# Kernel optimization log

Measured on AMD Instinct MI355X. Metric: run time of the kernel, lower is better.

## Reference

```python
import jax, jax.numpy as jnp
import numpy as np
from jax import lax

C = 256
HEADS = 8
HD = C // HEADS  # 32
D = 32  # max(L=32, C//16)
KERNELS = [1, 3, 5, 7]
EPS = 1e-5


def setup_inputs() -> dict:
    key = jax.random.key(0)
    ks = jax.random.split(key, 16)
    inp = {
        'x': jax.random.normal(ks[0], (8, C, 32, 32), jnp.float32),
        'qkv_w': jax.random.normal(ks[1], (3 * C, C), jnp.float32) * 0.05,
        'out_w': jax.random.normal(ks[2], (C, C), jnp.float32) * 0.05,
        'conv_w1': jax.random.normal(ks[3], (C, C, 1, 1), jnp.float32) * 0.05,
        'conv_w3': jax.random.normal(ks[4], (C, C, 3, 3), jnp.float32) * 0.05,
        'conv_w5': jax.random.normal(ks[5], (C, C, 5, 5), jnp.float32) * 0.05,
        'conv_w7': jax.random.normal(ks[6], (C, C, 7, 7), jnp.float32) * 0.05,
        'conv_b': jax.random.normal(ks[7], (4, C), jnp.float32) * 0.05,
        'bn_gamma': jax.random.uniform(ks[8], (4, C), jnp.float32, 0.5, 1.5),
        'bn_beta': jax.random.normal(ks[9], (4, C), jnp.float32) * 0.05,
        'bn_mean': jax.random.normal(ks[10], (4, C), jnp.float32) * 0.05,
        'bn_var': jax.random.uniform(ks[11], (4, C), jnp.float32, 0.5, 1.5),
        'fc_w': jax.random.normal(ks[12], (D, C), jnp.float32) * 0.05,
        'fc_b': jax.random.normal(ks[13], (D,), jnp.float32) * 0.05,
        'fcs_w': jax.random.normal(ks[14], (4, C, D), jnp.float32) * 0.05,
        'fcs_b': jax.random.normal(ks[15], (4, C), jnp.float32) * 0.05,
    }
    return inp


def _conv_bn_relu(x, w, b, g, beta, m, v):
    k = w.shape[-1]
    y = lax.conv_general_dilated(
        x, w, window_strides=(1, 1), padding=[(k // 2, k // 2)] * 2,
        dimension_numbers=('NCHW', 'OIHW', 'NCHW'))
    y = y + b[None, :, None, None]
    inv = g / jnp.sqrt(v + EPS)  # eval-mode batchnorm
    y = y * inv[None, :, None, None] + (beta - m * inv)[None, :, None, None]
    return jax.nn.relu(y)


def reference(x, qkv_w, out_w, conv_w1, conv_w3, conv_w5, conv_w7, conv_b,
              bn_gamma, bn_beta, bn_mean, bn_var, fc_w, fc_b, fcs_w, fcs_b):
    bsz, ch, ht, wd = x.shape
    n = ht * wd
    xf = x.reshape(bsz, ch, n)
    qkv = jnp.einsum('oc,bcn->bon', qkv_w, xf)  # [b, 3C, N] (1x1 conv)
    q, k, v = jnp.split(qkv, 3, axis=1)
    q = q.reshape(bsz, HEADS, HD, n)
    k = k.reshape(bsz, HEADS, HD, n)
    v = v.reshape(bsz, HEADS, HD, n)
    scale = 1.0 / np.sqrt(HD)
    scores = jnp.einsum('bhdi,bhdj->bhij', q, k) * scale  # [b,h,N,N]
    probs = jax.nn.softmax(scores, axis=-1)
    ctx = jnp.einsum('bhij,bhdj->bhdi', probs, v)  # [b,h,hd,N]
    ctx = ctx.reshape(bsz, ch, ht, wd)
    out = jnp.einsum('oc,bcn->bon', out_w, ctx.reshape(bsz, ch, n)).reshape(bsz, ch, ht, wd)

    ws = [conv_w1, conv_w3, conv_w5, conv_w7]
    feats = jnp.stack([
        _conv_bn_relu(out, ws[i], conv_b[i], bn_gamma[i], bn_beta[i], bn_mean[i], bn_var[i])
        for i in range(4)
    ], axis=0)  # [4, b, C, H, W]
    U = feats.sum(axis=0)
    S = U.mean(axis=(-2, -1))  # [b, C]
    Z = S @ fc_w.T + fc_b  # [b, D]
    logits = jnp.einsum('kcd,bd->kbc', fcs_w, Z) + fcs_b[:, None, :]  # [4,b,C]
    attn = jax.nn.softmax(logits, axis=0)[:, :, :, None, None]  # softmax over kernel branches
    V = (attn * feats).sum(axis=0)  # [b, C, H, W]
    return V
```

## Files before the change

### kernel.cpp

```cpp
#include <hip/hip_runtime.h>
#include <math.h>


typedef __attribute__((ext_vector_type(8))) short bf16x8;
typedef __attribute__((ext_vector_type(4))) float f32x4;

__device__ __forceinline__ ushort f2bf(float f) {
  uint32_t u = __float_as_uint(f);
  u += 0x7fffu + ((u >> 16) & 1u);
  return (ushort)(u >> 16);
}

__device__ __forceinline__ uint cvt_pk(float lo, float hi) {
  uint r;
  asm volatile("v_cvt_pk_bf16_f32 %0, %1, %2" : "=v"(r) : "v"(lo), "v"(hi));
  return r;
}


template <int KK>
__device__ __forceinline__ void repack_dev(const float* __restrict__ src,
                                           ushort* __restrict__ dst, int M, int co,
                                           char* smraw) {
  ushort(*t)[KK + 1] = (ushort(*)[KK + 1])smraw;
  int tid = threadIdx.x;
  for (int idx = tid; idx < 256 * KK; idx += 256) {
    int ci = idx / KK, k = idx - ci * KK;
    t[ci][k] = f2bf(src[(size_t)co * 256 * KK + idx]);
  }
  __syncthreads();
  for (int idx = tid; idx < 256 * KK; idx += 256) {
    int k = idx >> 8, ci = idx & 255;
    dst[((size_t)k * M + co) * 256 + ci] = t[ci][k];
  }
}

__device__ __forceinline__ void pad_dev(const float* __restrict__ src,
                                        ushort* __restrict__ dst, int y, int b,
                                        char* smraw) {
  ushort(*t)[258] = (ushort(*)[258])smraw;
  int tid = threadIdx.x;
  for (int u = 0; u < 32; ++u) {
    int idx = u * 256 + tid;
    int c = idx >> 5, p = idx & 31;
    t[p][c] = f2bf(src[(((size_t)b * 256 + c) << 10) + (y << 5) + p]);
  }
  __syncthreads();
  for (int u = 0; u < 32; ++u) {
    int idx = u * 256 + tid;
    int p = idx >> 8, c = idx & 255;
    dst[(((size_t)b * 38 + y + 3) * 38 + p + 3) * 256 + c] = t[p][c];
  }
}

__global__ __launch_bounds__(256) void prep_all(
    const float* __restrict__ qkv_w, const float* __restrict__ out_w,
    const float* __restrict__ cw1, const float* __restrict__ cw3,
    const float* __restrict__ cw5, const float* __restrict__ cw7,
    ushort* __restrict__ Wq, ushort* __restrict__ Wo, ushort* __restrict__ Wc,
    const float* __restrict__ x, ushort* __restrict__ P1,
    const float* __restrict__ cb, const float* __restrict__ g,
    const float* __restrict__ be, const float* __restrict__ mn,
    const float* __restrict__ v, float* __restrict__ binv, float* __restrict__ bb2) {
  __shared__ __align__(16) char sm[25600];
  int gx = blockIdx.x;
  if (gx < 768) repack_dev<1>(qkv_w, Wq, 768, gx, sm);
  else if (gx < 1024) repack_dev<1>(out_w, Wo, 256, gx - 768, sm);
  else if (gx < 1280) repack_dev<1>(cw1, Wc, 256, gx - 1024, sm);
  else if (gx < 1536) repack_dev<9>(cw3, Wc + 65536, 256, gx - 1280, sm);
  else if (gx < 1792) repack_dev<25>(cw5, Wc + 655360, 256, gx - 1536, sm);
  else if (gx < 2048) repack_dev<49>(cw7, Wc + 2293760, 256, gx - 1792, sm);
  else if (gx < 2304) pad_dev(x, P1, (gx - 2048) & 31, (gx - 2048) >> 5, sm);
  else if (gx == 2304) {
    int tid = threadIdx.x;
#pragma unroll
    for (int u = 0; u < 4; ++u) {
      int i = u * 256 + tid;
      float inv = g[i] * rsqrtf(v[i] + 1e-5f);
      binv[i] = inv;
      bb2[i] = be[i] + (cb[i] - mn[i]) * inv;
    }
  } else {
    int z = gx - 2305;
    int b = z >> 3;
    int part = z & 7;
    uint4* b4 = (uint4*)(P1 + (size_t)b * 369664);
    uint4 z4; z4.x = z4.y = z4.z = z4.w = 0u;
    for (int q = 0; q < 7; ++q) {
      int idx = q * 256 + threadIdx.x;
      if (idx < 1680) {
        int uidx = part * 1680 + idx;
        int p = uidx >> 5, ch = uidx & 31;
        int y, xx;
        if (p < 114) { y = p / 38; xx = p - y * 38; }
        else if (p < 306) {
          int r = p - 114; int ry = r / 6; int xi = r - ry * 6;
          y = 3 + ry; xx = xi < 3 ? xi : xi + 32;
        } else {
          int r = p - 306; int ry = r / 38; y = 35 + ry; xx = r - ry * 38;
        }
        b4[(y * 38 + xx) * 32 + ch] = z4;
      }
    }
  }
}

template <int MODE>
__device__ __forceinline__ void conv_core(
    const ushort* __restrict__ W, const ushort* __restrict__ X,
    float* __restrict__ outF, ushort* __restrict__ outU,
    int M, int KS, int b, int co0, int pxt, int cs0, int cs1, bool accum,
    char* smem) {
  const int R = KS >> 1;
  const int NT = KS * KS;
  const int NR = 4 + 2 * R;
  const int NPIX = NR * 38;
  char* Bs = smem;
  char* As = smem + 24320;
  const int tid = threadIdx.x;
  const int w = tid >> 6, l = tid & 63, lr = l & 15, sg = l >> 4;
  const int y0 = pxt * 4;
  const ushort* Xb = X + ((size_t)b * 38 + (y0 + 3 - R)) * 38 * 256;

  f32x4 acc[4][4] = {};

  auto stageA = [&](int t, int ci0, int bufsel) {
    const ushort* Wt = W + ((size_t)t * M + co0) * 256 + ci0;
    char* dbase = As + (bufsel << 13) + (w << 11);
#pragma unroll
    for (int u = 0; u < 2; ++u) {
      int idx16 = (w * 2 + u) * 64 + l;
      int co = idx16 >> 2, s = idx16 & 3;
      const ushort* src = Wt + (size_t)co * 256 + ((s ^ ((co >> 1) & 3)) << 3);
      __builtin_amdgcn_global_load_lds(
          (const __attribute__((address_space(1))) void*)src,
          (__attribute__((address_space(3))) void*)(dbase + (u << 10)), 16, 0, 0);
    }
  };

  int g = 0;
  stageA(0, cs0 << 5, 0);
  const int u_stg = (NPIX * 4 + 255) >> 8;
  for (int cs = cs0; cs < cs1; ++cs) {
    int ci0 = cs << 5;
    for (int u = 0; u < u_stg; ++u) {
      int idx = (u << 8) + tid;
      if (idx < NPIX * 4) {
        int pix = idx >> 2, s = idx & 3;
        int pr = pix / 38, pc = pix - pr * 38;
        const ushort* srcp = Xb + ((size_t)(pr * 38 + pc)) * 256 + ci0 +
                             ((s ^ ((pc >> 1) & 3)) << 3);
        __builtin_amdgcn_global_load_lds(
            (const __attribute__((address_space(1))) void*)srcp,
            (__attribute__((address_space(3))) void*)(Bs + (u << 12) + (w << 10)),
            16, 0, 0);
      }
    }
    __syncthreads();
    int dy = 0, dx = 0;
    for (int t = 0; t < NT; ++t) {
      bool staged = true;
      if (t + 1 < NT) stageA(t + 1, ci0, (g + 1) & 1);
      else if (cs + 1 < cs1) stageA(0, ci0 + 32, (g + 1) & 1);
      else staged = false;
      if (staged)
        asm volatile("s_waitcnt vmcnt(2)\n\ts_barrier" ::: "memory");
      else
        asm volatile("s_waitcnt vmcnt(0)\n\ts_barrier" ::: "memory");

      bf16x8 af[4], bfr[4];
      char* Ab = As + ((g & 1) << 13);
#pragma unroll
      for (int fa = 0; fa < 4; ++fa) {
        int co = (w & 1) * 64 + fa * 16 + lr;
        af[fa] = *(const bf16x8*)(Ab + (co << 6) + ((sg ^ ((co >> 1) & 3)) << 4));
      }
      int rowbase = (w >> 1) * 2 + dy;
      int cbase = dx + 3 - R + lr;
#pragma unroll
      for (int fp = 0; fp < 4; ++fp) {
        int lrow = rowbase + (fp >> 1);
        int pc = cbase + ((fp & 1) << 4);
        bfr[fp] = *(const bf16x8*)(Bs + ((lrow * 38 + pc) << 6) +
                                   ((sg ^ ((pc >> 1) & 3)) << 4));
      }
      __builtin_amdgcn_s_setprio(1);
#pragma unroll
      for (int fa = 0; fa < 4; ++fa)
#pragma unroll
        for (int fp = 0; fp < 4; ++fp)
          acc[fa][fp] = __builtin_amdgcn_mfma_f32_16x16x32_bf16(
              af[fa], bfr[fp], acc[fa][fp], 0, 0, 0);
      __builtin_amdgcn_s_setprio(0);
      ++g;
      if (++dx == KS) { dx = 0; ++dy; }
      asm volatile("s_barrier" ::: "memory");
    }
  }
  int coB = co0 + (w & 1) * 64;
  int pxB = pxt * 128 + (w >> 1) * 64;
#pragma unroll
  for (int fa = 0; fa < 4; ++fa) {
#pragma unroll
    for (int fp = 0; fp < 4; ++fp) {
      int px = pxB + (fp >> 1) * 32 + (fp & 1) * 16 + lr;
      int cobase = coB + fa * 16 + 4 * sg;
      f32x4 v4 = acc[fa][fp];
      if (MODE == 2) {
#pragma unroll
        for (int r = 0; r < 4; ++r) {
          int co = cobase + r;
          float* dst = &outF[((size_t)b * M + co) * 1024 + px];
          if (accum) unsafeAtomicAdd(dst, v4[r]);
          else *dst = v4[r];
        }
      } else if (MODE == 1) {
        int y = px >> 5, x = px & 31;
        ushort* dst = outU + ((size_t)(b * 38 + y + 3) * 38 + x + 3) * 256 + cobase;
        *(uint*)dst = cvt_pk(v4[0], v4[1]);
        *(uint*)(dst + 2) = cvt_pk(v4[2], v4[3]);
      } else {
        if (coB < 256) {
          int h = cobase >> 5, d = cobase & 31;
          ushort* dst = outU + ((size_t)(b * 8 + h) * 1024 + px) * 32 + d;
          const float sc = 0.17677669529663687f;
          *(uint*)dst = cvt_pk(v4[0] * sc, v4[1] * sc);
          *(uint*)(dst + 2) = cvt_pk(v4[2] * sc, v4[3] * sc);
        } else if (coB < 512) {
          int c2 = cobase - 256;
          int h = c2 >> 5, d = c2 & 31;
          ushort* dst = outU + 2097152 + ((size_t)(b * 8 + h) * 1024 + px) * 32 + d;
          *(uint*)dst = cvt_pk(v4[0], v4[1]);
          *(uint*)(dst + 2) = cvt_pk(v4[2], v4[3]);
        } else {
          int c2 = cobase - 512;
#pragma unroll
          for (int r = 0; r < 4; ++r)
            outU[4194304 + ((size_t)(b * 256 + c2 + r)) * 1024 + px] = f2bf(v4[r]);
        }
      }
    }
  }
}

__global__ __launch_bounds__(256, 2) void gemm_qkv(const ushort* __restrict__ W,
                                                   const ushort* __restrict__ X,
                                                   ushort* __restrict__ U) {
  __shared__ __align__(16) char smem[40704];
  int cot = blockIdx.x >> 3, pxt = blockIdx.x & 7, b = blockIdx.y;
  conv_core<0>(W, X, nullptr, U, 768, 1, b, cot * 128, pxt, 0, 8, false, smem);
}

__global__ __launch_bounds__(256, 2) void gemm_oproj(const ushort* __restrict__ W,
                                                     const ushort* __restrict__ X,
                                                     ushort* __restrict__ U,
                                                     float* __restrict__ fz) {
  __shared__ __align__(16) char smem[40704];
  int cot = blockIdx.x >> 3, pxt = blockIdx.x & 7, b = blockIdx.y;
  conv_core<1>(W, X, nullptr, U, 256, 1, b, cot * 128, pxt, 0, 8, false, smem);
  int blk = blockIdx.y * 16 + blockIdx.x;
  float4* dst = (float4*)fz + (size_t)blk * 12288;
  float4 z4 = {0.f, 0.f, 0.f, 0.f};
#pragma unroll
  for (int q = 0; q < 48; ++q) dst[q * 256 + threadIdx.x] = z4;
}

__global__ __launch_bounds__(256, 4) void conv_fused(const ushort* __restrict__ Wc,
                                                     const ushort* __restrict__ X,
                                                     float* __restrict__ feats) {
  __shared__ __align__(16) char smem[40704];
  int gx = blockIdx.x;
  int sub = gx & 127;
  int pxt = sub & 7, cot = (sub >> 3) & 1, b = sub >> 4;
  int br, cs0, cs1;
  if (gx < 512) {
    br = 3; int ch = gx >> 7; cs0 = ch * 2; cs1 = cs0 + 2;
  } else if (gx < 768) {
    br = 2; int ch = (gx >> 7) & 1; cs0 = ch * 4; cs1 = cs0 + 4;
  } else {
    br = 1; int ch = (gx >> 7) & 1; cs0 = ch * 4; cs1 = cs0 + 4;
  }
  const int ksarr[4] = {1, 3, 5, 7};
  const int wofs[4] = {0, 65536, 655360, 2293760};
  conv_core<2>(Wc + wofs[br], X, feats + (size_t)br * 2097152, nullptr, 256,
               ksarr[br], b, cot * 128, pxt, cs0, cs1, true, smem);
  if (gx >= 768 && gx < 896) {
    __syncthreads();
    conv_core<2>(Wc, X, feats, nullptr, 256, 1, b, cot * 128, pxt, 0, 8, false,
                 smem);
  }
}

__global__ __launch_bounds__(256, 2) void flash_attn(const ushort* __restrict__ QKV,
                                                     ushort* __restrict__ P2out) {
  __shared__ __align__(16) char smem[16384];
  const int tid = threadIdx.x, w = tid >> 6, l = tid & 63, lr = l & 15, sg = l >> 4;
  char* Ps = smem + (w << 12);
  int bh = blockIdx.y, b = bh >> 3, h = bh & 7;
  const ushort* QT = QKV + (size_t)bh * 32768;
  const ushort* KT = QKV + 2097152 + (size_t)bh * 32768;
  const ushort* VT = QKV + 4194304 + (size_t)(b * 256 + h * 32) * 1024;
  int ibase = blockIdx.x * 128 + w * 32;

  bf16x8 qf[2];
#pragma unroll
  for (int i16 = 0; i16 < 2; ++i16)
    qf[i16] = *(const bf16x8*)(QT + ((size_t)(ibase + i16 * 16 + lr)) * 32 + sg * 8);

  f32x4 oacc[4] = {};
  float mrow[2] = {-3e30f, -3e30f};
  float lrow[2] = {0.f, 0.f};

  const ushort* Krow = KT + (size_t)lr * 32 + sg * 8;
  const ushort* Vrow = VT + (size_t)lr * 1024 + sg * 8;

  bf16x8 k0[4], v0[4], k1[4], v1[4];
  auto LK = [&](int jb, bf16x8* kf) {
#pragma unroll
    for (int jt = 0; jt < 4; ++jt)
      kf[jt] = *(const bf16x8*)(Krow + ((size_t)jb + jt * 16) * 32);
  };
  auto LV = [&](int jb, bf16x8* vf) {
#pragma unroll
    for (int d16 = 0; d16 < 2; ++d16)
#pragma unroll
      for (int h2 = 0; h2 < 2; ++h2)
        vf[d16 * 2 + h2] =
            *(const bf16x8*)(Vrow + (size_t)d16 * 16384 + jb + h2 * 32);
  };

  auto body = [&](int jb, bf16x8* kc, bf16x8* vc, bf16x8* kn, bf16x8* vn) {
    if (jb + 64 < 1024) { LK(jb + 64, kn); LV(jb + 64, vn); }
    f32x4 sac[2][4] = {};
#pragma unroll
    for (int i16 = 0; i16 < 2; ++i16)
#pragma unroll
      for (int jt = 0; jt < 4; ++jt)
        sac[i16][jt] = __builtin_amdgcn_mfma_f32_16x16x32_bf16(
            kc[jt], qf[i16], sac[i16][jt], 0, 0, 0);

#pragma unroll
    for (int i16 = 0; i16 < 2; ++i16) {
      float tmax = sac[i16][0][0];
#pragma unroll
      for (int jt = 0; jt < 4; ++jt)
#pragma unroll
        for (int r = 0; r < 4; ++r) tmax = fmaxf(tmax, sac[i16][jt][r]);
      tmax = fmaxf(tmax, __shfl_xor(tmax, 16));
      tmax = fmaxf(tmax, __shfl_xor(tmax, 32));
      float mnew = fmaxf(mrow[i16], tmax);
      float fac = __expf(mrow[i16] - mnew);
      mrow[i16] = mnew;
      float psum = 0.f;
      int i = i16 * 16 + lr;
      char* prow = Ps + i * 128;
#pragma unroll
      for (int jt = 0; jt < 4; ++jt) {
        float p0 = __expf(sac[i16][jt][0] - mnew);
        float p1 = __expf(sac[i16][jt][1] - mnew);
        float p2 = __expf(sac[i16][jt][2] - mnew);
        float p3 = __expf(sac[i16][jt][3] - mnew);
        psum += (p0 + p1) + (p2 + p3);
        int j0 = jt * 16 + sg * 4;
        uint* dst = (uint*)(prow + (((j0 >> 3) ^ (i & 7)) << 4) + ((j0 & 7) << 1));
        dst[0] = cvt_pk(p0, p1);
        dst[1] = cvt_pk(p2, p3);
      }
      lrow[i16] = lrow[i16] * fac + psum;
#pragma unroll
      for (int d16 = 0; d16 < 2; ++d16)
#pragma unroll
        for (int r = 0; r < 4; ++r) oacc[d16 * 2 + i16][r] *= fac;
    }
    asm volatile("s_waitcnt lgkmcnt(0)" ::: "memory");

#pragma unroll
    for (int h2 = 0; h2 < 2; ++h2) {
      bf16x8 pf[2];
#pragma unroll
      for (int i16 = 0; i16 < 2; ++i16) {
        int i = i16 * 16 + lr;
        pf[i16] = *(const bf16x8*)(Ps + i * 128 + ((((h2 << 2) + sg) ^ (i & 7)) << 4));
      }
#pragma unroll
      for (int d16 = 0; d16 < 2; ++d16)
#pragma unroll
        for (int i16 = 0; i16 < 2; ++i16)
          oacc[d16 * 2 + i16] = __builtin_amdgcn_mfma_f32_16x16x32_bf16(
              vc[d16 * 2 + h2], pf[i16], oacc[d16 * 2 + i16], 0, 0, 0);
    }
  };

  LK(0, k0);
  LV(0, v0);
#pragma unroll 1
  for (int jb = 0; jb < 1024; jb += 128) {
    body(jb, k0, v0, k1, v1);
    body(jb + 64, k1, v1, k0, v0);
  }

  float linv[2];
#pragma unroll
  for (int i16 = 0; i16 < 2; ++i16) {
    float lt = lrow[i16];
    lt += __shfl_xor(lt, 16);
    lt += __shfl_xor(lt, 32);
    linv[i16] = 1.0f / lt;
  }
#pragma unroll
  for (int i16 = 0; i16 < 2; ++i16) {
    int i = ibase + i16 * 16 + lr;
    int y = i >> 5, x = i & 31;
    ushort* dst0 = P2out + ((size_t)(b * 38 + y + 3) * 38 + x + 3) * 256 + h * 32 + sg * 4;
#pragma unroll
    for (int d16 = 0; d16 < 2; ++d16) {
      f32x4 v = oacc[d16 * 2 + i16];
      ushort* dst = dst0 + d16 * 16;
      *(uint*)dst = cvt_pk(v[0] * linv[i16], v[1] * linv[i16]);
      *(uint*)(dst + 2) = cvt_pk(v[2] * linv[i16], v[3] * linv[i16]);
    }
  }
}

__global__ __launch_bounds__(256) void reduce_s(const float* __restrict__ feats,
                                                const float* __restrict__ binv,
                                                const float* __restrict__ bb2,
                                                float* __restrict__ S) {
  int bc = blockIdx.x;
  int c = bc & 255;
  const float4* p4 = (const float4*)feats + (size_t)bc * 256;
  float s = 0;
#pragma unroll
  for (int k = 0; k < 4; ++k) {
    float bi = binv[k * 256 + c], bo = bb2[k * 256 + c];
    float4 v = p4[(size_t)k * 524288 + threadIdx.x];
    s += fmaxf(fmaf(v.x, bi, bo), 0.f) + fmaxf(fmaf(v.y, bi, bo), 0.f) +
         fmaxf(fmaf(v.z, bi, bo), 0.f) + fmaxf(fmaf(v.w, bi, bo), 0.f);
  }
  __shared__ float red[256];
  red[threadIdx.x] = s;
  __syncthreads();
  for (int off = 128; off > 0; off >>= 1) {
    if (threadIdx.x < off) red[threadIdx.x] += red[threadIdx.x + off];
    __syncthreads();
  }
  if (threadIdx.x == 0) S[bc] = red[0] * (1.0f / 1024.0f);
}

__global__ __launch_bounds__(256) void fc_attn_k(
    const float* __restrict__ S, const float* __restrict__ fc_w,
    const float* __restrict__ fc_b, const float* __restrict__ fcs_w,
    const float* __restrict__ fcs_b, float* __restrict__ attnw) {
  int b = blockIdx.x;
  __shared__ float Ss[256];
  __shared__ float Zs[32];
  int tid = threadIdx.x;
  Ss[tid] = S[b * 256 + tid];
  __syncthreads();
  if (tid < 32) {
    float z = fc_b[tid];
    for (int c = 0; c < 256; ++c) z += Ss[c] * fc_w[tid * 256 + c];
    Zs[tid] = z;
  }
  __syncthreads();
  int c = tid;
  float lg[4];
#pragma unroll
  for (int k = 0; k < 4; ++k) {
    float v = fcs_b[k * 256 + c];
    const float* wp = &fcs_w[((size_t)k * 256 + c) * 32];
#pragma unroll
    for (int d = 0; d < 32; ++d) v += wp[d] * Zs[d];
    lg[k] = v;
  }
  float m = fmaxf(fmaxf(lg[0], lg[1]), fmaxf(lg[2], lg[3]));
  float e0 = __expf(lg[0] - m), e1 = __expf(lg[1] - m);
  float e2 = __expf(lg[2] - m), e3 = __expf(lg[3] - m);
  float inv = 1.0f / (e0 + e1 + e2 + e3);
  attnw[(0 * 8 + b) * 256 + c] = e0 * inv;
  attnw[(1 * 8 + b) * 256 + c] = e1 * inv;
  attnw[(2 * 8 + b) * 256 + c] = e2 * inv;
  attnw[(3 * 8 + b) * 256 + c] = e3 * inv;
}

__global__ __launch_bounds__(256) void combine_k(const float* __restrict__ feats,
                                                 const float* __restrict__ attnw,
                                                 const float* __restrict__ binv,
                                                 const float* __restrict__ bb2,
                                                 float* __restrict__ out) {
  size_t i4 = (size_t)blockIdx.x * 256 + threadIdx.x;
  int c = (int)((i4 >> 8) & 255);
  int b = (int)(i4 >> 16);
  float4 s = {0.f, 0.f, 0.f, 0.f};
#pragma unroll
  for (int k = 0; k < 4; ++k) {
    float bi = binv[k * 256 + c], bo = bb2[k * 256 + c];
    float aw = attnw[(k * 8 + b) * 256 + c];
    float4 v = ((const float4*)feats)[(size_t)k * 524288 + i4];
    s.x += aw * fmaxf(fmaf(v.x, bi, bo), 0.f);
    s.y += aw * fmaxf(fmaf(v.y, bi, bo), 0.f);
    s.z += aw * fmaxf(fmaf(v.z, bi, bo), 0.f);
    s.w += aw * fmaxf(fmaf(v.w, bi, bo), 0.f);
  }
  ((float4*)out)[i4] = s;
}

extern "C" void kernel_launch(void* const* d_in, const int* in_sizes, int n_in,
                              void* d_out, int out_size, void* d_ws, size_t ws_size,
                              hipStream_t stream) {
  (void)in_sizes; (void)n_in; (void)out_size; (void)ws_size;
  const float* x      = (const float*)d_in[0];
  const float* qkv_w  = (const float*)d_in[1];
  const float* out_w  = (const float*)d_in[2];
  const float* cw1    = (const float*)d_in[3];
  const float* cw3    = (const float*)d_in[4];
  const float* cw5    = (const float*)d_in[5];
  const float* cw7    = (const float*)d_in[6];
  const float* conv_b = (const float*)d_in[7];
  const float* bn_g   = (const float*)d_in[8];
  const float* bn_b   = (const float*)d_in[9];
  const float* bn_m   = (const float*)d_in[10];
  const float* bn_v   = (const float*)d_in[11];
  const float* fc_w   = (const float*)d_in[12];
  const float* fc_b   = (const float*)d_in[13];
  const float* fcs_w  = (const float*)d_in[14];
  const float* fcs_b  = (const float*)d_in[15];

  char*  wsb   = (char*)d_ws;
  float* wsf   = (float*)d_ws;
  ushort* QKVb = (ushort*)d_ws;
  float* feats = wsf;
  float* S     = wsf + 10485760;
  float* attnw = wsf + 10487808;
  ushort* P1   = (ushort*)(wsb + 41984000);
  ushort* P2   = (ushort*)(wsb + 47898624);
  ushort* Wq   = (ushort*)(wsb + 53813248);
  ushort* Wo   = (ushort*)(wsb + 54206464);
  ushort* Wc   = (ushort*)(wsb + 54337536);
  float* binv  = (float*)(wsb + 65347584);
  float* bb2   = (float*)(wsb + 65351680);
  float* out   = (float*)d_out;

  prep_all<<<2369, 256, 0, stream>>>(qkv_w, out_w, cw1, cw3, cw5, cw7, Wq, Wo, Wc,
                                     x, P1, conv_b, bn_g, bn_b, bn_m, bn_v,
                                     binv, bb2);

  gemm_qkv<<<dim3(48, 8), 256, 0, stream>>>(Wq, P1, QKVb);
  flash_attn<<<dim3(8, 64), 256, 0, stream>>>(QKVb, P2);
  gemm_oproj<<<dim3(16, 8), 256, 0, stream>>>(Wo, P2, P1, (float*)(wsb + 8388608));
  conv_fused<<<dim3(1024), 256, 0, stream>>>(Wc, P1, feats);

  reduce_s<<<2048, 256, 0, stream>>>(feats, binv, bb2, S);
  fc_attn_k<<<8, 256, 0, stream>>>(S, fc_w, fc_b, fcs_w, fcs_b, attnw);
  combine_k<<<2048, 256, 0, stream>>>(feats, attnw, binv, bb2, out);
}
```

Measured before the change: 200.9 us.

## Load conv weight fragments directly from global into registers, drop LDS double buffer

The weight (A) operand is now read by each lane straight from global memory into MFMA registers, replacing the double-buffered LDS staging with its per-tap barriers. This shrinks shared memory from about 40 KB to 24 KB per block and removes two barriers per tap, which may allow more resident blocks. The cost is that weight loads are no longer prefetched: each tap's global load sits right before its MFMAs, and loads are uncoalesced and repeated across waves, so latency may be exposed.

```diff
diff --git a/kernel.cpp b/kernel.cpp
--- a/kernel.cpp
+++ b/kernel.cpp
@@ -116,33 +116,46 @@
   const int NR = 4 + 2 * R;
   const int NPIX = NR * 38;
   char* Bs = smem;
-  char* As = smem + 24320;
   const int tid = threadIdx.x;
   const int w = tid >> 6, l = tid & 63, lr = l & 15, sg = l >> 4;
   const int y0 = pxt * 4;
   const ushort* Xb = X + ((size_t)b * 38 + (y0 + 3 - R)) * 38 * 256;
+  const ushort* Wlane = W + ((size_t)(co0 + (w & 1) * 64 + lr)) * 256 + sg * 8;
 
   f32x4 acc[4][4] = {};
-
-  auto stageA = [&](int t, int ci0, int bufsel) {
-    const ushort* Wt = W + ((size_t)t * M + co0) * 256 + ci0;
-    char* dbase = As + (bufsel << 13) + (w << 11);
-#pragma unroll
-    for (int u = 0; u < 2; ++u) {
-      int idx16 = (w * 2 + u) * 64 + l;
-      int co = idx16 >> 2, s = idx16 & 3;
-      const ushort* src = Wt + (size_t)co * 256 + ((s ^ ((co >> 1) & 3)) << 3);
-      __builtin_amdgcn_global_load_lds(
-          (const __attribute__((address_space(1))) void*)src,
-          (__attribute__((address_space(3))) void*)(dbase + (u << 10)), 16, 0, 0);
-    }
+  bf16x8 af[4];
+
+  auto LA = [&](int t, int ci0) {
+#pragma unroll
+    for (int fa = 0; fa < 4; ++fa)
+      af[fa] = *(const bf16x8*)(Wlane + (size_t)(t * M + fa * 16) * 256 + ci0);
   };
 
-  int g = 0;
-  stageA(0, cs0 << 5, 0);
+  auto TAP = [&](int dy, int dx) {
+    bf16x8 bfr[4];
+    int rowbase = (w >> 1) * 2 + dy;
+    int cbase = dx + 3 - R + lr;
+#pragma unroll
+    for (int fp = 0; fp < 4; ++fp) {
+      int lrow = rowbase + (fp >> 1);
+      int pc = cbase + ((fp & 1) << 4);
+      bfr[fp] = *(const bf16x8*)(Bs + ((lrow * 38 + pc) << 6) +
+                                 ((sg ^ ((pc >> 1) & 3)) << 4));
+    }
+    __builtin_amdgcn_s_setprio(1);
+#pragma unroll
+    for (int fa = 0; fa < 4; ++fa)
+#pragma unroll
+      for (int fp = 0; fp < 4; ++fp)
+        acc[fa][fp] = __builtin_amdgcn_mfma_f32_16x16x32_bf16(
+            af[fa], bfr[fp], acc[fa][fp], 0, 0, 0);
+    __builtin_amdgcn_s_setprio(0);
+  };
+
   const int u_stg = (NPIX * 4 + 255) >> 8;
   for (int cs = cs0; cs < cs1; ++cs) {
     int ci0 = cs << 5;
+    if (cs > cs0) __syncthreads();
     for (int u = 0; u < u_stg; ++u) {
       int idx = (u << 8) + tid;
       if (idx < NPIX * 4) {
@@ -158,43 +171,11 @@
     }
     __syncthreads();
     int dy = 0, dx = 0;
+#pragma unroll 1
     for (int t = 0; t < NT; ++t) {
-      bool staged = true;
-      if (t + 1 < NT) stageA(t + 1, ci0, (g + 1) & 1);
-      else if (cs + 1 < cs1) stageA(0, ci0 + 32, (g + 1) & 1);
-      else staged = false;
-      if (staged)
-        asm volatile("s_waitcnt vmcnt(2)\n\ts_barrier" ::: "memory");
-      else
-        asm volatile("s_waitcnt vmcnt(0)\n\ts_barrier" ::: "memory");
-
-      bf16x8 af[4], bfr[4];
-      char* Ab = As + ((g & 1) << 13);
-#pragma unroll
-      for (int fa = 0; fa < 4; ++fa) {
-        int co = (w & 1) * 64 + fa * 16 + lr;
-        af[fa] = *(const bf16x8*)(Ab + (co << 6) + ((sg ^ ((co >> 1) & 3)) << 4));
-      }
-      int rowbase = (w >> 1) * 2 + dy;
-      int cbase = dx + 3 - R + lr;
-#pragma unroll
-      for (int fp = 0; fp < 4; ++fp) {
-        int lrow = rowbase + (fp >> 1);
-        int pc = cbase + ((fp & 1) << 4);
-        bfr[fp] = *(const bf16x8*)(Bs + ((lrow * 38 + pc) << 6) +
-                                   ((sg ^ ((pc >> 1) & 3)) << 4));
-      }
-      __builtin_amdgcn_s_setprio(1);
-#pragma unroll
-      for (int fa = 0; fa < 4; ++fa)
-#pragma unroll
-        for (int fp = 0; fp < 4; ++fp)
-          acc[fa][fp] = __builtin_amdgcn_mfma_f32_16x16x32_bf16(
-              af[fa], bfr[fp], acc[fa][fp], 0, 0, 0);
-      __builtin_amdgcn_s_setprio(0);
-      ++g;
+      LA(t, ci0);
+      TAP(dy, dx);
       if (++dx == KS) { dx = 0; ++dy; }
-      asm volatile("s_barrier" ::: "memory");
     }
   }
   int coB = co0 + (w & 1) * 64;
@@ -246,7 +227,7 @@
 __global__ __launch_bounds__(256, 2) void gemm_qkv(const ushort* __restrict__ W,
                                                    const ushort* __restrict__ X,
                                                    ushort* __restrict__ U) {
-  __shared__ __align__(16) char smem[40704];
+  __shared__ __align__(16) char smem[24320];
   int cot = blockIdx.x >> 3, pxt = blockIdx.x & 7, b = blockIdx.y;
   conv_core<0>(W, X, nullptr, U, 768, 1, b, cot * 128, pxt, 0, 8, false, smem);
 }
@@ -255,7 +236,7 @@
                                                      const ushort* __restrict__ X,
                                                      ushort* __restrict__ U,
                                                      float* __restrict__ fz) {
-  __shared__ __align__(16) char smem[40704];
+  __shared__ __align__(16) char smem[24320];
   int cot = blockIdx.x >> 3, pxt = blockIdx.x & 7, b = blockIdx.y;
   conv_core<1>(W, X, nullptr, U, 256, 1, b, cot * 128, pxt, 0, 8, false, smem);
   int blk = blockIdx.y * 16 + blockIdx.x;
@@ -268,7 +249,7 @@
 __global__ __launch_bounds__(256, 4) void conv_fused(const ushort* __restrict__ Wc,
                                                      const ushort* __restrict__ X,
                                                      float* __restrict__ feats) {
-  __shared__ __align__(16) char smem[40704];
+  __shared__ __align__(16) char smem[24320];
   int gx = blockIdx.x;
   int sub = gx & 127;
   int pxt = sub & 7, cot = (sub >> 3) & 1, b = sub >> 4;
```

New measurement: 295.5 us. 1.47x slower.

## Fuse tail reduce, FC attention, and combine into one kernel with grid barrier

Applied to the files above, without the earlier changes.

Replaces the three tail kernels (channel mean reduction, FC/softmax attention, weighted combine) with one persistent-style kernel. Each block keeps its BN+ReLU'd branch values in registers, publishes its channel mean, waits at a global atomic barrier, then computes the attention weights and writes the output. This removes the second full read of the four-branch feats buffer and two kernel launches. In exchange it relies on all 1024 blocks being co-resident for the spin barrier, which has a guard timeout, and each block recomputes the small FC layer redundantly. It also simplifies the 1x1 weight repack so it skips the shared-memory transpose.

```diff
diff --git a/kernel.cpp b/kernel.cpp
--- a/kernel.cpp
+++ b/kernel.cpp
@@ -22,16 +22,22 @@
 __device__ __forceinline__ void repack_dev(const float* __restrict__ src,
                                            ushort* __restrict__ dst, int M, int co,
                                            char* smraw) {
-  ushort(*t)[KK + 1] = (ushort(*)[KK + 1])smraw;
-  int tid = threadIdx.x;
-  for (int idx = tid; idx < 256 * KK; idx += 256) {
-    int ci = idx / KK, k = idx - ci * KK;
-    t[ci][k] = f2bf(src[(size_t)co * 256 * KK + idx]);
-  }
-  __syncthreads();
-  for (int idx = tid; idx < 256 * KK; idx += 256) {
-    int k = idx >> 8, ci = idx & 255;
-    dst[((size_t)k * M + co) * 256 + ci] = t[ci][k];
+  if constexpr (KK == 1) {
+    int tid = threadIdx.x;
+    dst[(size_t)co * 256 + tid] = f2bf(src[(size_t)co * 256 + tid]);
+    return;
+  } else {
+    ushort(*t)[KK + 1] = (ushort(*)[KK + 1])smraw;
+    int tid = threadIdx.x;
+    for (int idx = tid; idx < 256 * KK; idx += 256) {
+      int ci = idx / KK, k = idx - ci * KK;
+      t[ci][k] = f2bf(src[(size_t)co * 256 * KK + idx]);
+    }
+    __syncthreads();
+    for (int idx = tid; idx < 256 * KK; idx += 256) {
+      int k = idx >> 8, ci = idx & 255;
+      dst[((size_t)k * M + co) * 256 + ci] = t[ci][k];
+    }
   }
 }
 
@@ -254,7 +260,8 @@
 __global__ __launch_bounds__(256, 2) void gemm_oproj(const ushort* __restrict__ W,
                                                      const ushort* __restrict__ X,
                                                      ushort* __restrict__ U,
-                                                     float* __restrict__ fz) {
+                                                     float* __restrict__ fz,
+                                                     uint* __restrict__ bar) {
   __shared__ __align__(16) char smem[40704];
   int cot = blockIdx.x >> 3, pxt = blockIdx.x & 7, b = blockIdx.y;
   conv_core<1>(W, X, nullptr, U, 256, 1, b, cot * 128, pxt, 0, 8, false, smem);
@@ -263,6 +270,8 @@
   float4 z4 = {0.f, 0.f, 0.f, 0.f};
 #pragma unroll
   for (int q = 0; q < 48; ++q) dst[q * 256 + threadIdx.x] = z4;
+  if (blk == 0 && threadIdx.x == 0)
+    __hip_atomic_store(bar, 0u, __ATOMIC_RELAXED, __HIP_MEMORY_SCOPE_AGENT);
 }
 
 __global__ __launch_bounds__(256, 4) void conv_fused(const ushort* __restrict__ Wc,
@@ -422,87 +431,105 @@
   }
 }
 
-__global__ __launch_bounds__(256) void reduce_s(const float* __restrict__ feats,
-                                                const float* __restrict__ binv,
-                                                const float* __restrict__ bb2,
-                                                float* __restrict__ S) {
-  int bc = blockIdx.x;
-  int c = bc & 255;
-  const float4* p4 = (const float4*)feats + (size_t)bc * 256;
-  float s = 0;
-#pragma unroll
-  for (int k = 0; k < 4; ++k) {
-    float bi = binv[k * 256 + c], bo = bb2[k * 256 + c];
-    float4 v = p4[(size_t)k * 524288 + threadIdx.x];
-    s += fmaxf(fmaf(v.x, bi, bo), 0.f) + fmaxf(fmaf(v.y, bi, bo), 0.f) +
-         fmaxf(fmaf(v.z, bi, bo), 0.f) + fmaxf(fmaf(v.w, bi, bo), 0.f);
-  }
+__global__ __launch_bounds__(256, 4) void fused_tail(
+    const float* __restrict__ feats, const float* __restrict__ binv,
+    const float* __restrict__ bb2, const float* __restrict__ fc_w,
+    const float* __restrict__ fc_b, const float* __restrict__ fcs_w,
+    const float* __restrict__ fcs_b, float* __restrict__ S,
+    uint* __restrict__ bar, float* __restrict__ out) {
   __shared__ float red[256];
-  red[threadIdx.x] = s;
-  __syncthreads();
-  for (int off = 128; off > 0; off >>= 1) {
-    if (threadIdx.x < off) red[threadIdx.x] += red[threadIdx.x + off];
-    __syncthreads();
-  }
-  if (threadIdx.x == 0) S[bc] = red[0] * (1.0f / 1024.0f);
-}
-
-__global__ __launch_bounds__(256) void fc_attn_k(
-    const float* __restrict__ S, const float* __restrict__ fc_w,
-    const float* __restrict__ fc_b, const float* __restrict__ fcs_w,
-    const float* __restrict__ fcs_b, float* __restrict__ attnw) {
-  int b = blockIdx.x;
   __shared__ float Ss[256];
   __shared__ float Zs[32];
-  int tid = threadIdx.x;
-  Ss[tid] = S[b * 256 + tid];
+  const int tid = threadIdx.x;
+  const int bc0 = blockIdx.x * 2;
+  float4 ya[4], yb[4];
+
+#pragma unroll
+  for (int half = 0; half < 2; ++half) {
+    int bc = bc0 + half;
+    int c = bc & 255;
+    const float4* p4 = (const float4*)feats + (size_t)bc * 256;
+    float s = 0.f;
+    float4* y = half ? yb : ya;
+#pragma unroll
+    for (int k = 0; k < 4; ++k) {
+      float bi = binv[k * 256 + c], bo = bb2[k * 256 + c];
+      float4 v = p4[(size_t)k * 524288 + tid];
+      float4 r;
+      r.x = fmaxf(fmaf(v.x, bi, bo), 0.f);
+      r.y = fmaxf(fmaf(v.y, bi, bo), 0.f);
+      r.z = fmaxf(fmaf(v.z, bi, bo), 0.f);
+      r.w = fmaxf(fmaf(v.w, bi, bo), 0.f);
+      y[k] = r;
+      s += (r.x + r.y) + (r.z + r.w);
+    }
+    red[tid] = s;
+    __syncthreads();
+    for (int off = 128; off > 0; off >>= 1) {
+      if (tid < off) red[tid] += red[tid + off];
+      __syncthreads();
+    }
+    if (tid == 0)
+      __hip_atomic_store(&S[bc], red[0] * (1.0f / 1024.0f), __ATOMIC_RELAXED,
+                         __HIP_MEMORY_SCOPE_AGENT);
+    __syncthreads();
+  }
+
+  __threadfence();
+  __syncthreads();
+  if (tid == 0) {
+    __hip_atomic_fetch_add(bar, 1u, __ATOMIC_ACQ_REL, __HIP_MEMORY_SCOPE_AGENT);
+    long guard = 0;
+    while (__hip_atomic_load(bar, __ATOMIC_ACQUIRE, __HIP_MEMORY_SCOPE_AGENT) <
+               1024u &&
+           guard < (1L << 26)) {
+      __builtin_amdgcn_s_sleep(8);
+      ++guard;
+    }
+  }
+  __syncthreads();
+
+  const int b = bc0 >> 8;
+  Ss[tid] = __hip_atomic_load(&S[b * 256 + tid], __ATOMIC_RELAXED,
+                              __HIP_MEMORY_SCOPE_AGENT);
   __syncthreads();
   if (tid < 32) {
     float z = fc_b[tid];
-    for (int c = 0; c < 256; ++c) z += Ss[c] * fc_w[tid * 256 + c];
+    const float* wp = &fc_w[tid * 256];
+    for (int c = 0; c < 256; ++c) z += Ss[c] * wp[c];
     Zs[tid] = z;
   }
   __syncthreads();
-  int c = tid;
-  float lg[4];
-#pragma unroll
-  for (int k = 0; k < 4; ++k) {
-    float v = fcs_b[k * 256 + c];
-    const float* wp = &fcs_w[((size_t)k * 256 + c) * 32];
-#pragma unroll
-    for (int d = 0; d < 32; ++d) v += wp[d] * Zs[d];
-    lg[k] = v;
-  }
-  float m = fmaxf(fmaxf(lg[0], lg[1]), fmaxf(lg[2], lg[3]));
-  float e0 = __expf(lg[0] - m), e1 = __expf(lg[1] - m);
-  float e2 = __expf(lg[2] - m), e3 = __expf(lg[3] - m);
-  float inv = 1.0f / (e0 + e1 + e2 + e3);
-  attnw[(0 * 8 + b) * 256 + c] = e0 * inv;
-  attnw[(1 * 8 + b) * 256 + c] = e1 * inv;
-  attnw[(2 * 8 + b) * 256 + c] = e2 * inv;
-  attnw[(3 * 8 + b) * 256 + c] = e3 * inv;
-}
-
-__global__ __launch_bounds__(256) void combine_k(const float* __restrict__ feats,
-                                                 const float* __restrict__ attnw,
-                                                 const float* __restrict__ binv,
-                                                 const float* __restrict__ bb2,
-                                                 float* __restrict__ out) {
-  size_t i4 = (size_t)blockIdx.x * 256 + threadIdx.x;
-  int c = (int)((i4 >> 8) & 255);
-  int b = (int)(i4 >> 16);
-  float4 s = {0.f, 0.f, 0.f, 0.f};
-#pragma unroll
-  for (int k = 0; k < 4; ++k) {
-    float bi = binv[k * 256 + c], bo = bb2[k * 256 + c];
-    float aw = attnw[(k * 8 + b) * 256 + c];
-    float4 v = ((const float4*)feats)[(size_t)k * 524288 + i4];
-    s.x += aw * fmaxf(fmaf(v.x, bi, bo), 0.f);
-    s.y += aw * fmaxf(fmaf(v.y, bi, bo), 0.f);
-    s.z += aw * fmaxf(fmaf(v.z, bi, bo), 0.f);
-    s.w += aw * fmaxf(fmaf(v.w, bi, bo), 0.f);
-  }
-  ((float4*)out)[i4] = s;
+
+#pragma unroll
+  for (int half = 0; half < 2; ++half) {
+    int bc = bc0 + half;
+    int c = bc & 255;
+    const float4* y = half ? yb : ya;
+    float lg[4];
+#pragma unroll
+    for (int k = 0; k < 4; ++k) {
+      float v = fcs_b[k * 256 + c];
+      const float* wp = &fcs_w[((size_t)k * 256 + c) * 32];
+#pragma unroll
+      for (int d = 0; d < 32; ++d) v += wp[d] * Zs[d];
+      lg[k] = v;
+    }
+    float m = fmaxf(fmaxf(lg[0], lg[1]), fmaxf(lg[2], lg[3]));
+    float e0 = __expf(lg[0] - m), e1 = __expf(lg[1] - m);
+    float e2 = __expf(lg[2] - m), e3 = __expf(lg[3] - m);
+    float inv = 1.0f / (e0 + e1 + e2 + e3);
+    float aw[4] = {e0 * inv, e1 * inv, e2 * inv, e3 * inv};
+    float4 o = {0.f, 0.f, 0.f, 0.f};
+#pragma unroll
+    for (int k = 0; k < 4; ++k) {
+      o.x += aw[k] * y[k].x;
+      o.y += aw[k] * y[k].y;
+      o.z += aw[k] * y[k].z;
+      o.w += aw[k] * y[k].w;
+    }
+    ((float4*)out)[(size_t)bc * 256 + tid] = o;
+  }
 }
 
 extern "C" void kernel_launch(void* const* d_in, const int* in_sizes, int n_in,
@@ -531,7 +558,7 @@
   ushort* QKVb = (ushort*)d_ws;
   float* feats = wsf;
   float* S     = wsf + 10485760;
-  float* attnw = wsf + 10487808;
+  uint*  bar   = (uint*)(wsb + 41951232);
   ushort* P1   = (ushort*)(wsb + 41984000);
   ushort* P2   = (ushort*)(wsb + 47898624);
   ushort* Wq   = (ushort*)(wsb + 53813248);
@@ -547,10 +574,10 @@
 
   gemm_qkv<<<dim3(48, 8), 256, 0, stream>>>(Wq, P1, QKVb);
   flash_attn<<<dim3(8, 64), 256, 0, stream>>>(QKVb, P2);
-  gemm_oproj<<<dim3(16, 8), 256, 0, stream>>>(Wo, P2, P1, (float*)(wsb + 8388608));
+  gemm_oproj<<<dim3(16, 8), 256, 0, stream>>>(Wo, P2, P1,
+                                              (float*)(wsb + 8388608), bar);
   conv_fused<<<dim3(1024), 256, 0, stream>>>(Wc, P1, feats);
 
-  reduce_s<<<2048, 256, 0, stream>>>(feats, binv, bb2, S);
-  fc_attn_k<<<8, 256, 0, stream>>>(S, fc_w, fc_b, fcs_w, fcs_b, attnw);
-  combine_k<<<2048, 256, 0, stream>>>(feats, attnw, binv, bb2, out);
-}
+  fused_tail<<<1024, 256, 0, stream>>>(feats, binv, bb2, fc_w, fc_b, fcs_w,
+                                       fcs_b, S, bar, out);
+}
```

New measurement: 295.5 us. 1.47x slower.
